# Kernel optimization log

Hardware: AMD Instinct MI355X
Metric: run time of the kernel (lower is better)

## Reference

```python
import jax, jax.numpy as jnp
import numpy as np

B, N, T, E, R, NSEL = 128, 1000, 50, 32000, 4, 500
F0, CF = 3, 20
FS = 2 * CF + F0  # 43


def _conv(x, w, b):
    # NCHW valid conv, stride 1
    y = jax.lax.conv_general_dilated(x, w, (1, 1), 'VALID',
                                     dimension_numbers=('NCHW', 'OIHW', 'NCHW'))
    return y + b[None, :, None, None]


def setup_inputs() -> dict:
    key = jax.random.key(0)
    ks = jax.random.split(key, 20)
    s = 0.1
    return {
        'observation': jax.random.normal(ks[0], (B, F0, N, T), jnp.float32),
        'last_action': jax.random.uniform(ks[1], (B, NSEL + 1), jnp.float32),
        'w_s1': jax.random.normal(ks[2], (3, 3, 1, 3), jnp.float32) * s,
        'b_s1': jax.random.normal(ks[3], (3,), jnp.float32) * s,
        'w_s2': jax.random.normal(ks[4], (20, 3, 1, 48), jnp.float32) * s,
        'b_s2': jax.random.normal(ks[5], (20,), jnp.float32) * s,
        'w_m1': jax.random.normal(ks[6], (3, 3, 1, 21), jnp.float32) * s,
        'b_m1': jax.random.normal(ks[7], (3,), jnp.float32) * s,
        'w_m2': jax.random.normal(ks[8], (20, 3, 1, 30), jnp.float32) * s,
        'b_m2': jax.random.normal(ks[9], (20,), jnp.float32) * s,
        'w_rel': jax.random.normal(ks[10], (R, FS, FS), jnp.float32) * s,
        'w_root': jax.random.normal(ks[11], (FS, FS), jnp.float32) * s,
        'b_g': jax.random.normal(ks[12], (FS,), jnp.float32) * s,
        'w_fin': jax.random.normal(ks[13], (1, 2 * FS + 1, 1, 1), jnp.float32) * s,
        'b_fin': jax.random.normal(ks[14], (1,), jnp.float32) * s,
        'edge_index': jax.random.randint(ks[15], (2, E), 0, N, jnp.int64) if jax.config.jax_enable_x64 else jax.random.randint(ks[15], (2, E), 0, N).astype(jnp.int32),
        'edge_type': jax.random.randint(ks[16], (E,), 0, R).astype(jnp.int32),
        'nodes_to_select': jnp.sort(jax.random.randint(ks[17], (NSEL,), 0, N)).astype(jnp.int32),
    }


def reference(observation, last_action, w_s1, b_s1, w_s2, b_s2, w_m1, b_m1,
              w_m2, b_m2, w_rel, w_root, b_g, w_fin, b_fin,
              edge_index, edge_type, nodes_to_select):
    # temporal feature extraction
    short = jax.nn.relu(_conv(jax.nn.relu(_conv(observation, w_s1, b_s1)), w_s2, b_s2))
    mid = jax.nn.relu(_conv(jax.nn.relu(_conv(observation, w_m1, b_m1)), w_m2, b_m2))
    long = jax.nn.relu(jnp.max(observation, axis=3, keepdims=True))
    temporal = jnp.concatenate([short, mid, long], axis=1)  # [B, 43, N, 1]

    x = temporal[:, :, :, 0].transpose(0, 2, 1)  # [B, N, F]

    # RGCNConv with per-relation mean aggregation
    src, dst = edge_index[0], edge_index[1]
    xw = jnp.einsum('bnf,rfg->bnrg', x, w_rel)        # [B, N, R, F]
    msgs = xw[:, src, edge_type, :]                   # [B, E, F] gather
    seg = dst * R + edge_type                         # per (node, relation) segment
    agg = jax.vmap(lambda m: jax.ops.segment_sum(m, seg, num_segments=N * R))(msgs)
    cnt = jax.ops.segment_sum(jnp.ones((E,), x.dtype), seg, num_segments=N * R)
    inv = jnp.where(cnt > 0, 1.0 / cnt, 0.0)
    agg = (agg * inv[None, :, None]).reshape(B, N, R, FS).sum(axis=2)
    gout = jax.nn.leaky_relu(agg + x @ w_root + b_g, 0.01)  # [B, N, F]

    graph_features = gout.transpose(0, 2, 1)[..., None]     # [B, F, N, 1]
    feat = jnp.concatenate([temporal, graph_features], axis=1)  # [B, 86, N, 1]
    feat = feat[:, :, nodes_to_select, :]                       # [B, 86, NSEL, 1]
    last_stocks = last_action[:, 1:].reshape(B, 1, NSEL, 1)
    feat = jnp.concatenate([last_stocks, feat], axis=1)         # [B, 87, NSEL, 1]

    o = jnp.einsum('bcn,oc->bon', feat[..., 0], w_fin[:, :, 0, 0]) + b_fin[None, :, None]
    o = jnp.concatenate([jnp.zeros((B, 1, 1), o.dtype), o], axis=2)[:, 0, :]  # [B, NSEL+1]
    return jax.nn.softmax(o / 1.0, axis=-1)
```

## Files before the change

### kernel.cpp

```cpp
#include <hip/hip_runtime.h>
#include <hip/hip_fp16.h>
#include <math.h>

#define Bn 128
#define Nn 1000
#define Tn 50
#define En 32000
#define Rn 4
#define FSn 43
#define NSELn 500
#define NFtot (Nn * FSn)

__global__ __launch_bounds__(512) void k_temporal(
    const float* __restrict__ obs,
    const float* __restrict__ w_s1, const float* __restrict__ b_s1,
    const float* __restrict__ w_s2, const float* __restrict__ b_s2,
    const float* __restrict__ w_m1, const float* __restrict__ b_m1,
    const float* __restrict__ w_m2, const float* __restrict__ b_m2,
    float* __restrict__ x)
{
    __shared__ float lds[3 * 64 * 51];

    const int b     = blockIdx.x;
    const int tile0 = blockIdx.y * 64;
    const int tid   = threadIdx.x;
    const int lane  = tid & 63;
    const int w     = __builtin_amdgcn_readfirstlane(tid >> 6);
    const int nrows = (Nn - tile0) < 64 ? (Nn - tile0) : 64;

    for (int c = 0; c < 3; ++c) {
        const float* srcp = obs + ((size_t)(b * 3 + c) * Nn + tile0) * Tn;
        for (int idx = tid; idx < nrows * Tn; idx += 512) {
            const int r = idx / Tn;
            const int t = idx - r * Tn;
            lds[(c * 64 + r) * 51 + t] = srcp[idx];
        }
    }
    __syncthreads();

    float acc[20];
    float mx0 = -1e30f, mx1 = -1e30f, mx2 = -1e30f;

    if (w < 3) {
        #pragma unroll
        for (int o = 0; o < 20; ++o) acc[o] = (w == 0) ? b_s2[o] : 0.f;

        const float s10 = b_s1[0], s11 = b_s1[1], s12 = b_s1[2];
        const int t0 = w * 16;

        #pragma unroll 1
        for (int t = t0; t < t0 + 16; ++t) {
            float ov[9];
            #pragma unroll
            for (int c = 0; c < 3; ++c)
                #pragma unroll
                for (int d = 0; d < 3; ++d)
                    ov[c * 3 + d] = lds[(c * 64 + lane) * 51 + t + d];

            float v0 = s10, v1 = s11, v2 = s12;
            #pragma unroll
            for (int c = 0; c < 3; ++c) {
                v0 += ov[c * 3 + 0] * w_s1[(0 * 3 + c) * 3 + 0]
                    + ov[c * 3 + 1] * w_s1[(0 * 3 + c) * 3 + 1]
                    + ov[c * 3 + 2] * w_s1[(0 * 3 + c) * 3 + 2];
                v1 += ov[c * 3 + 0] * w_s1[(1 * 3 + c) * 3 + 0]
                    + ov[c * 3 + 1] * w_s1[(1 * 3 + c) * 3 + 1]
                    + ov[c * 3 + 2] * w_s1[(1 * 3 + c) * 3 + 2];
                v2 += ov[c * 3 + 0] * w_s1[(2 * 3 + c) * 3 + 0]
                    + ov[c * 3 + 1] * w_s1[(2 * 3 + c) * 3 + 1]
                    + ov[c * 3 + 2] * w_s1[(2 * 3 + c) * 3 + 2];
            }
            v0 = fmaxf(v0, 0.f); v1 = fmaxf(v1, 0.f); v2 = fmaxf(v2, 0.f);
            #pragma unroll
            for (int o = 0; o < 20; ++o) {
                acc[o] += v0 * w_s2[(o * 3 + 0) * 48 + t]
                        + v1 * w_s2[(o * 3 + 1) * 48 + t]
                        + v2 * w_s2[(o * 3 + 2) * 48 + t];
            }
        }

        const int rb0 = (0 * 64 + lane) * 51;
        const int rb1 = (1 * 64 + lane) * 51;
        const int rb2 = (2 * 64 + lane) * 51;
        const int l0 = (w == 0) ? 0 : (w == 1) ? 17 : 34;
        const int l1 = (w == 0) ? 17 : (w == 1) ? 34 : 50;
        #pragma unroll 1
        for (int t = l0; t < l1; ++t) {
            mx0 = fmaxf(mx0, lds[rb0 + t]);
            mx1 = fmaxf(mx1, lds[rb1 + t]);
            mx2 = fmaxf(mx2, lds[rb2 + t]);
        }
    } else {
        #pragma unroll
        for (int o = 0; o < 20; ++o) acc[o] = (w == 3) ? b_m2[o] : 0.f;

        const float m10 = b_m1[0], m11 = b_m1[1], m12 = b_m1[2];
        const int t0 = (w - 3) * 6;

        #pragma unroll 1
        for (int t = t0; t < t0 + 6; ++t) {
            float v0 = m10, v1 = m11, v2 = m12;
            #pragma unroll
            for (int c = 0; c < 3; ++c) {
                const int base = (c * 64 + lane) * 51 + t;
                float p0 = 0.f, p1 = 0.f, p2 = 0.f;
                #pragma unroll
                for (int d = 0; d < 21; ++d) {
                    const float ov = lds[base + d];
                    p0 += ov * w_m1[(0 * 3 + c) * 21 + d];
                    p1 += ov * w_m1[(1 * 3 + c) * 21 + d];
                    p2 += ov * w_m1[(2 * 3 + c) * 21 + d];
                }
                v0 += p0; v1 += p1; v2 += p2;
            }
            v0 = fmaxf(v0, 0.f); v1 = fmaxf(v1, 0.f); v2 = fmaxf(v2, 0.f);
            #pragma unroll
            for (int o = 0; o < 20; ++o) {
                acc[o] += v0 * w_m2[(o * 3 + 0) * 30 + t]
                        + v1 * w_m2[(o * 3 + 1) * 30 + t]
                        + v2 * w_m2[(o * 3 + 2) * 30 + t];
            }
        }
    }

    __syncthreads();
    if (w == 1 || w == 2) {
        float* r = lds + (w - 1) * 1472 + lane;
        #pragma unroll
        for (int o = 0; o < 20; ++o) r[o * 64] = acc[o];
        r[20 * 64] = mx0;
        r[21 * 64] = mx1;
        r[22 * 64] = mx2;
    } else if (w >= 4) {
        float* r = lds + 2944 + (w - 4) * 1280 + lane;
        #pragma unroll
        for (int o = 0; o < 20; ++o) r[o * 64] = acc[o];
    }
    __syncthreads();

    if (lane < nrows) {
        float* xp = x + ((size_t)b * Nn + tile0 + lane) * FSn;
        if (w == 0) {
            #pragma unroll
            for (int o = 0; o < 20; ++o) {
                const int a = o * 64 + lane;
                xp[o] = fmaxf(acc[o] + lds[a] + lds[1472 + a], 0.f);
            }
            {
                const int a0 = 20 * 64 + lane, a1 = 21 * 64 + lane, a2 = 22 * 64 + lane;
                xp[40] = fmaxf(fmaxf(mx0, fmaxf(lds[a0], lds[1472 + a0])), 0.f);
                xp[41] = fmaxf(fmaxf(mx1, fmaxf(lds[a1], lds[1472 + a1])), 0.f);
                xp[42] = fmaxf(fmaxf(mx2, fmaxf(lds[a2], lds[1472 + a2])), 0.f);
            }
        } else if (w == 3) {
            #pragma unroll
            for (int o = 0; o < 20; ++o) {
                const int a = 2944 + o * 64 + lane;
                xp[20 + o] = fmaxf(acc[o] + lds[a] + lds[a + 1280]
                                          + lds[a + 2560] + lds[a + 3840], 0.f);
            }
        }
    }
}

__global__ __launch_bounds__(256) void k_transpose(const float* __restrict__ x,
                                                   __half* __restrict__ xT)
{
    __shared__ float tile[64][129];
    const int c0  = blockIdx.x * 64;
    const int tid = threadIdx.x;

    const int j  = tid & 63;
    const int bs = tid >> 6;
    for (int bb = bs; bb < Bn; bb += 4) {
        int c = c0 + j;
        if (c < NFtot) tile[j][bb] = x[(size_t)bb * NFtot + c];
    }
    __syncthreads();

    const int b  = tid & 127;
    for (int jj = (tid >> 7); jj < 64; jj += 2) {
        int c = c0 + jj;
        if (c < NFtot) xT[(size_t)c * Bn + b] = __float2half(tile[jj][b]);
    }
}

__global__ void k_count(const int* __restrict__ ei, const int* __restrict__ et,
                        int* __restrict__ cnt)
{
    int e = blockIdx.x * blockDim.x + threadIdx.x;
    if (e < En) {
        int dst = ei[En + e];
        atomicAdd(&cnt[dst * Rn + et[e]], 1);
    }
}

__global__ __launch_bounds__(1024) void k_scan(const int* __restrict__ cnt,
                                               int* __restrict__ off)
{
    __shared__ int sums[1024];
    int tid = threadIdx.x;
    int base = tid * 4;
    int c[4];
    int ts = 0;
    #pragma unroll
    for (int k = 0; k < 4; ++k) {
        int i = base + k;
        c[k] = (i < Nn * Rn) ? cnt[i] : 0;
        ts += c[k];
    }
    sums[tid] = ts;
    __syncthreads();
    for (int d = 1; d < 1024; d <<= 1) {
        int t = 0;
        if (tid >= d) t = sums[tid - d];
        __syncthreads();
        sums[tid] += t;
        __syncthreads();
    }
    int excl = sums[tid] - ts;
    #pragma unroll
    for (int k = 0; k < 4; ++k) {
        int i = base + k;
        off[i] = excl;
        excl += c[k];
    }
}

__global__ void k_fill(const int* __restrict__ ei, const int* __restrict__ et,
                       const int* __restrict__ off, int* __restrict__ pos,
                       int* __restrict__ csr)
{
    int e = blockIdx.x * blockDim.x + threadIdx.x;
    if (e < En) {
        int src = ei[e];
        int dst = ei[En + e];
        int seg = dst * Rn + et[e];
        int p = atomicAdd(&pos[seg], 1);
        csr[off[seg] + p] = src;
    }
}

__global__ __launch_bounds__(256) void k_graph(
    const __half* __restrict__ xT,
    const float* __restrict__ w_rel, const float* __restrict__ w_root,
    const float* __restrict__ b_g,
    const float* __restrict__ w_fin, const float* __restrict__ b_fin,
    const float* __restrict__ la,
    const int* __restrict__ csr, const int* __restrict__ off,
    const int* __restrict__ cnt, const int* __restrict__ sel,
    float* __restrict__ logitT)
{
    __shared__ __align__(16) char smem[22016 + 2048 + 32];
    __half* ab    = (__half*)smem;
    int*    srcs  = (int*)(smem + 22016);
    int*    scnt  = (int*)(smem + 22016 + 2048);
    int*    tcnt  = scnt + 4;
    float*  red   = (float*)smem;

    const int i   = blockIdx.x >> 1;
    const int bh  = blockIdx.x & 1;
    const int dst = sel[i];
    const int tid = threadIdx.x;

    {
        const int r = tid >> 6;
        const int c = cnt[dst * Rn + r];
        const int o = off[dst * Rn + r];
        if ((tid & 63) == 0) { tcnt[r] = c; scnt[r] = (c < 128) ? c : 128; }
        #pragma unroll
        for (int j = (tid & 63); j < 128; j += 64)
            if (j < c) srcs[r * 128 + j] = csr[o + j];
    }
    __syncthreads();

    {
        const int r  = tid >> 6;
        const int fc = (tid >> 4) & 3;
        const int b2 = tid & 15;
        const int nk = (fc < 3) ? 11 : 10;

        float4 acc[11];
        #pragma unroll
        for (int k = 0; k < 11; ++k) acc[k] = make_float4(0.f, 0.f, 0.f, 0.f);

        const int cc = scnt[r];
        const float2* xT2 = (const float2*)xT;
        for (int j = 0; j < cc; ++j) {
            const int src = srcs[r * 128 + j];
            const float2* base = xT2 + (size_t)src * (FSn * 32)
                               + (size_t)fc * 32 + bh * 16 + b2;
            #pragma unroll
            for (int k = 0; k < 11; ++k) {
                if (k < nk) {
                    float2 raw = base[(size_t)k * 128];
                    const __half2 h0 = ((const __half2*)&raw)[0];
                    const __half2 h1 = ((const __half2*)&raw)[1];
                    const float2 f0 = __half22float2(h0);
                    const float2 f1 = __half22float2(h1);
                    acc[k].x += f0.x; acc[k].y += f0.y;
                    acc[k].z += f1.x; acc[k].w += f1.y;
                }
            }
        }

        const int  tc  = tcnt[r];
        const float inv = (tc > 0) ? 1.f / (float)tc : 0.f;
        float2* ab2 = (float2*)ab;
        #pragma unroll
        for (int k = 0; k < 11; ++k) {
            if (k < nk) {
                const int f = fc + 4 * k;
                float2 st;
                ((__half2*)&st)[0] = __floats2half2_rn(acc[k].x * inv, acc[k].y * inv);
                ((__half2*)&st)[1] = __floats2half2_rn(acc[k].z * inv, acc[k].w * inv);
                ab2[(r * FSn + f) * 16 + b2] = st;
            }
        }
    }
    __syncthreads();

    const int fs = tid >> 6;
    const int bL = tid & 63;
    const int b  = bh * 64 + bL;
    const int f0 = fs * 11;
    const int nf = (fs == 3) ? 10 : 11;

    float a[5][11];
    #pragma unroll
    for (int rr = 0; rr < 4; ++rr) {
        #pragma unroll
        for (int k = 0; k < 11; ++k)
            a[rr][k] = (k < nf) ? __half2float(ab[(rr * FSn + f0 + k) * 64 + bL]) : 0.f;
    }
    {
        const __half* xp = xT + ((size_t)dst * FSn + f0) * Bn + b;
        #pragma unroll
        for (int k = 0; k < 11; ++k)
            a[4][k] = (k < nf) ? __half2float(xp[(size_t)k * Bn]) : 0.f;
    }

    float accg[FSn];
    #pragma unroll
    for (int g = 0; g < FSn; ++g) accg[g] = 0.f;
    float psum = 0.f;

    #pragma unroll
    for (int k = 0; k < 11; ++k) {
        if (k < nf) {
            const int f = f0 + k;
            #pragma unroll
            for (int rr = 0; rr < 5; ++rr) {
                const float av = a[rr][k];
                const float* wrow = (rr < 4)
                    ? (w_rel + ((size_t)rr * FSn + f) * FSn)
                    : (w_root + (size_t)f * FSn);
                #pragma unroll
                for (int g = 0; g < FSn; ++g) accg[g] += av * wrow[g];
            }
            psum += a[4][k] * w_fin[1 + f];
        }
    }

    __syncthreads();

    if (fs == 3) {
        #pragma unroll
        for (int g = 0; g < FSn; ++g) red[g * 64 + bL] = accg[g];
        red[FSn * 64 + bL] = psum;
    }
    __syncthreads();
    if (fs == 2) {
        #pragma unroll
        for (int g = 0; g < FSn; ++g) red[g * 64 + bL] += accg[g];
        red[FSn * 64 + bL] += psum;
    }
    __syncthreads();
    if (fs == 1) {
        #pragma unroll
        for (int g = 0; g < FSn; ++g) red[g * 64 + bL] += accg[g];
        red[FSn * 64 + bL] += psum;
    }
    __syncthreads();
    if (fs == 0) {
        float logit = b_fin[0] + w_fin[0] * la[(size_t)b * (NSELn + 1) + 1 + i]
                    + psum + red[FSn * 64 + bL];
        #pragma unroll
        for (int g = 0; g < FSn; ++g) {
            float v = accg[g] + red[g * 64 + bL] + b_g[g];
            v = (v > 0.f) ? v : 0.01f * v;
            logit += v * w_fin[44 + g];
        }
        logitT[(size_t)i * Bn + b] = logit;
    }
}

__global__ __launch_bounds__(512) void k_softmax(const float* __restrict__ logitT,
                                                 float* __restrict__ out)
{
    __shared__ float red[512];
    const int b   = blockIdx.x;
    const int tid = threadIdx.x;

    const float l = (tid < NSELn) ? logitT[(size_t)tid * Bn + b] : -1e30f;
    red[tid] = l;
    __syncthreads();
    for (int s = 256; s > 0; s >>= 1) {
        if (tid < s) red[tid] = fmaxf(red[tid], red[tid + s]);
        __syncthreads();
    }
    const float m = fmaxf(red[0], 0.f);
    __syncthreads();

    const float e = (tid < NSELn) ? expf(l - m) : 0.f;
    red[tid] = e;
    __syncthreads();
    for (int s = 256; s > 0; s >>= 1) {
        if (tid < s) red[tid] += red[tid + s];
        __syncthreads();
    }
    const float e0  = expf(-m);
    const float inv = 1.f / (red[0] + e0);

    if (tid == 0) out[(size_t)b * (NSELn + 1)] = e0 * inv;
    if (tid < NSELn) out[(size_t)b * (NSELn + 1) + 1 + tid] = e * inv;
}

extern "C" void kernel_launch(void* const* d_in, const int* in_sizes, int n_in,
                              void* d_out, int out_size, void* d_ws, size_t ws_size,
                              hipStream_t stream)
{
    const float* obs    = (const float*)d_in[0];
    const float* la     = (const float*)d_in[1];
    const float* w_s1   = (const float*)d_in[2];
    const float* b_s1   = (const float*)d_in[3];
    const float* w_s2   = (const float*)d_in[4];
    const float* b_s2   = (const float*)d_in[5];
    const float* w_m1   = (const float*)d_in[6];
    const float* b_m1   = (const float*)d_in[7];
    const float* w_m2   = (const float*)d_in[8];
    const float* b_m2   = (const float*)d_in[9];
    const float* w_rel  = (const float*)d_in[10];
    const float* w_root = (const float*)d_in[11];
    const float* b_g    = (const float*)d_in[12];
    const float* w_fin  = (const float*)d_in[13];
    const float* b_fin  = (const float*)d_in[14];
    const int*   ei     = (const int*)d_in[15];
    const int*   et     = (const int*)d_in[16];
    const int*   sel    = (const int*)d_in[17];
    float*       out    = (float*)d_out;

    char* wsb     = (char*)d_ws;
    float* x      = (float*)wsb;
    __half* xTh   = (__half*)(wsb + 22016000);
    int*   cnt    = (int*)(wsb + 33024000);
    int*   pos    = cnt + 4096;
    int*   offb   = pos + 4096;
    int*   csr    = offb + 4096;
    float* logitT = (float*)(csr + 32000);

    hipMemsetAsync(cnt, 0, 2 * 4096 * sizeof(int), stream);
    hipLaunchKernelGGL(k_count, dim3((En + 255) / 256), dim3(256), 0, stream, ei, et, cnt);
    hipLaunchKernelGGL(k_scan,  dim3(1),   dim3(1024), 0, stream, cnt, offb);
    hipLaunchKernelGGL(k_fill,  dim3((En + 255) / 256), dim3(256), 0, stream, ei, et, offb, pos, csr);

    hipLaunchKernelGGL(k_temporal, dim3(Bn, (Nn + 63) / 64), dim3(512), 0, stream,
                       obs, w_s1, b_s1, w_s2, b_s2, w_m1, b_m1, w_m2, b_m2, x);

    hipLaunchKernelGGL(k_transpose, dim3((NFtot + 63) / 64), dim3(256), 0, stream, x, xTh);

    hipLaunchKernelGGL(k_graph, dim3(NSELn * 2), dim3(256), 0, stream,
                       xTh, w_rel, w_root, b_g, w_fin, b_fin, la,
                       csr, offb, cnt, sel, logitT);

    hipLaunchKernelGGL(k_softmax, dim3(Bn), dim3(512), 0, stream, logitT, out);
}
```

Measured before the change: 228.4 us.

## Split graph kernel into four batch quarters with 128-thread blocks and 16-byte gathers

The graph aggregation kernel now runs 4 blocks per selected node, each covering 32 batch entries with 128 threads, instead of 2 blocks of 256 threads covering 64 entries. The neighbour gather loads float4 (8 halves) per thread instead of float2, and the feature stride per thread changes from 4 to 8. The goals are more blocks for occupancy, smaller LDS use and wider memory transactions. In exchange, each row of 43 features is split among 4 lanes of 16 bytes, so gathers may coalesce less well, and the per-node setup and weight reads are repeated across twice as many blocks.

New measurement: 232.2 us. No clear change (+1.7%).

```diff
diff --git a/kernel.cpp b/kernel.cpp
--- a/kernel.cpp
+++ b/kernel.cpp
@@ -241,7 +241,7 @@
     }
 }
 
-__global__ __launch_bounds__(256) void k_graph(
+__global__ __launch_bounds__(128) void k_graph(
     const __half* __restrict__ xT,
     const float* __restrict__ w_rel, const float* __restrict__ w_root,
     const float* __restrict__ b_g,
@@ -251,78 +251,89 @@
     const int* __restrict__ cnt, const int* __restrict__ sel,
     float* __restrict__ logitT)
 {
-    __shared__ __align__(16) char smem[22016 + 2048 + 32];
+    __shared__ __align__(16) char smem[11008 + 2048 + 32];
     __half* ab    = (__half*)smem;
-    int*    srcs  = (int*)(smem + 22016);
-    int*    scnt  = (int*)(smem + 22016 + 2048);
+    int*    srcs  = (int*)(smem + 11008);
+    int*    scnt  = (int*)(smem + 11008 + 2048);
     int*    tcnt  = scnt + 4;
     float*  red   = (float*)smem;
 
-    const int i   = blockIdx.x >> 1;
-    const int bh  = blockIdx.x & 1;
+    const int i   = blockIdx.x >> 2;
+    const int bq  = blockIdx.x & 3;
     const int dst = sel[i];
     const int tid = threadIdx.x;
 
     {
-        const int r = tid >> 6;
+        const int r = tid >> 5;
         const int c = cnt[dst * Rn + r];
         const int o = off[dst * Rn + r];
-        if ((tid & 63) == 0) { tcnt[r] = c; scnt[r] = (c < 128) ? c : 128; }
-        #pragma unroll
-        for (int j = (tid & 63); j < 128; j += 64)
+        if ((tid & 31) == 0) { tcnt[r] = c; scnt[r] = (c < 128) ? c : 128; }
+        #pragma unroll
+        for (int j = (tid & 31); j < 128; j += 32)
             if (j < c) srcs[r * 128 + j] = csr[o + j];
     }
     __syncthreads();
 
     {
-        const int r  = tid >> 6;
-        const int fc = (tid >> 4) & 3;
-        const int b2 = tid & 15;
-        const int nk = (fc < 3) ? 11 : 10;
-
-        float4 acc[11];
-        #pragma unroll
-        for (int k = 0; k < 11; ++k) acc[k] = make_float4(0.f, 0.f, 0.f, 0.f);
+        const int r  = tid >> 5;
+        const int fc = (tid >> 2) & 7;
+        const int b4 = tid & 3;
+        const int nk = (fc < 3) ? 6 : 5;
+
+        float4 acl[6], ach[6];
+        #pragma unroll
+        for (int k = 0; k < 6; ++k) {
+            acl[k] = make_float4(0.f, 0.f, 0.f, 0.f);
+            ach[k] = make_float4(0.f, 0.f, 0.f, 0.f);
+        }
 
         const int cc = scnt[r];
-        const float2* xT2 = (const float2*)xT;
+        const float4* xT4 = (const float4*)xT;
+        #pragma unroll 2
         for (int j = 0; j < cc; ++j) {
             const int src = srcs[r * 128 + j];
-            const float2* base = xT2 + (size_t)src * (FSn * 32)
-                               + (size_t)fc * 32 + bh * 16 + b2;
-            #pragma unroll
-            for (int k = 0; k < 11; ++k) {
+            const float4* base = xT4 + (size_t)(src * FSn + fc) * 16 + bq * 4 + b4;
+            #pragma unroll
+            for (int k = 0; k < 6; ++k) {
                 if (k < nk) {
-                    float2 raw = base[(size_t)k * 128];
+                    float4 raw = base[(size_t)k * 128];
                     const __half2 h0 = ((const __half2*)&raw)[0];
                     const __half2 h1 = ((const __half2*)&raw)[1];
+                    const __half2 h2 = ((const __half2*)&raw)[2];
+                    const __half2 h3 = ((const __half2*)&raw)[3];
                     const float2 f0 = __half22float2(h0);
                     const float2 f1 = __half22float2(h1);
-                    acc[k].x += f0.x; acc[k].y += f0.y;
-                    acc[k].z += f1.x; acc[k].w += f1.y;
+                    const float2 f2 = __half22float2(h2);
+                    const float2 f3 = __half22float2(h3);
+                    acl[k].x += f0.x; acl[k].y += f0.y;
+                    acl[k].z += f1.x; acl[k].w += f1.y;
+                    ach[k].x += f2.x; ach[k].y += f2.y;
+                    ach[k].z += f3.x; ach[k].w += f3.y;
                 }
             }
         }
 
         const int  tc  = tcnt[r];
         const float inv = (tc > 0) ? 1.f / (float)tc : 0.f;
-        float2* ab2 = (float2*)ab;
-        #pragma unroll
-        for (int k = 0; k < 11; ++k) {
+        float4* ab4 = (float4*)ab;
+        #pragma unroll
+        for (int k = 0; k < 6; ++k) {
             if (k < nk) {
-                const int f = fc + 4 * k;
-                float2 st;
-                ((__half2*)&st)[0] = __floats2half2_rn(acc[k].x * inv, acc[k].y * inv);
-                ((__half2*)&st)[1] = __floats2half2_rn(acc[k].z * inv, acc[k].w * inv);
-                ab2[(r * FSn + f) * 16 + b2] = st;
-            }
-        }
-    }
-    __syncthreads();
-
-    const int fs = tid >> 6;
-    const int bL = tid & 63;
-    const int b  = bh * 64 + bL;
+                const int f = fc + 8 * k;
+                float4 st;
+                ((__half2*)&st)[0] = __floats2half2_rn(acl[k].x * inv, acl[k].y * inv);
+                ((__half2*)&st)[1] = __floats2half2_rn(acl[k].z * inv, acl[k].w * inv);
+                ((__half2*)&st)[2] = __floats2half2_rn(ach[k].x * inv, ach[k].y * inv);
+                ((__half2*)&st)[3] = __floats2half2_rn(ach[k].z * inv, ach[k].w * inv);
+                ab4[(r * FSn + f) * 4 + b4] = st;
+            }
+        }
+    }
+    __syncthreads();
+
+    const int fs = tid >> 5;
+    const int bL = tid & 31;
+    const int b  = bq * 32 + bL;
     const int f0 = fs * 11;
     const int nf = (fs == 3) ? 10 : 11;
 
@@ -331,7 +342,7 @@
     for (int rr = 0; rr < 4; ++rr) {
         #pragma unroll
         for (int k = 0; k < 11; ++k)
-            a[rr][k] = (k < nf) ? __half2float(ab[(rr * FSn + f0 + k) * 64 + bL]) : 0.f;
+            a[rr][k] = (k < nf) ? __half2float(ab[(rr * FSn + f0 + k) * 32 + bL]) : 0.f;
     }
     {
         const __half* xp = xT + ((size_t)dst * FSn + f0) * Bn + b;
@@ -366,28 +377,28 @@
 
     if (fs == 3) {
         #pragma unroll
-        for (int g = 0; g < FSn; ++g) red[g * 64 + bL] = accg[g];
-        red[FSn * 64 + bL] = psum;
+        for (int g = 0; g < FSn; ++g) red[g * 32 + bL] = accg[g];
+        red[FSn * 32 + bL] = psum;
     }
     __syncthreads();
     if (fs == 2) {
         #pragma unroll
-        for (int g = 0; g < FSn; ++g) red[g * 64 + bL] += accg[g];
-        red[FSn * 64 + bL] += psum;
+        for (int g = 0; g < FSn; ++g) red[g * 32 + bL] += accg[g];
+        red[FSn * 32 + bL] += psum;
     }
     __syncthreads();
     if (fs == 1) {
         #pragma unroll
-        for (int g = 0; g < FSn; ++g) red[g * 64 + bL] += accg[g];
-        red[FSn * 64 + bL] += psum;
+        for (int g = 0; g < FSn; ++g) red[g * 32 + bL] += accg[g];
+        red[FSn * 32 + bL] += psum;
     }
     __syncthreads();
     if (fs == 0) {
         float logit = b_fin[0] + w_fin[0] * la[(size_t)b * (NSELn + 1) + 1 + i]
-                    + psum + red[FSn * 64 + bL];
+                    + psum + red[FSn * 32 + bL];
         #pragma unroll
         for (int g = 0; g < FSn; ++g) {
-            float v = accg[g] + red[g * 64 + bL] + b_g[g];
+            float v = accg[g] + red[g * 32 + bL] + b_g[g];
             v = (v > 0.f) ? v : 0.01f * v;
             logit += v * w_fin[44 + g];
         }
@@ -469,7 +480,7 @@
 
     hipLaunchKernelGGL(k_transpose, dim3((NFtot + 63) / 64), dim3(256), 0, stream, x, xTh);
 
-    hipLaunchKernelGGL(k_graph, dim3(NSELn * 2), dim3(256), 0, stream,
+    hipLaunchKernelGGL(k_graph, dim3(NSELn * 4), dim3(128), 0, stream,
                        xTh, w_rel, w_root, b_g, w_fin, b_fin, la,
                        csr, offb, cnt, sel, logitT);
 
```
